# Kernel optimization log

Hardware: AMD Instinct MI355X
Metric: run time of the kernel (lower is better)

The kernel has to match this reference:

```python
import jax, jax.numpy as jnp
import numpy as np
import math

NUM_HEADS = 8
HEAD_DIM = 32  # num_units 256 / 8 heads
TIME_DIM = 8
NEG_BIG = -2.0 ** 32 + 1.0


def _ffn(x, W1, b1, W2, b2):
    # two-layer relu MLP: 1 -> time_dim -> time_dim
    h = jax.nn.relu(x @ W1 + b1)
    return jax.nn.relu(h @ W2 + b2)


def _time_gsm_kernel(t, pW1, pb1, pW2, pb2, sW1, sb1, sW2, sb2, bW1, bb1, bW2, bb2):
    # t: [B, L] timestamps -> kernel [B, L, L]
    tt = t[..., None]  # [B, L, 1]
    period = _ffn(tt, pW1, pb1, pW2, pb2)        # [B, L, td]
    qpq = (2.0 * math.pi) * period * tt           # [B, L, td]
    period_diff = qpq[:, :, None, :] - qpq[:, None, :, :]  # [B, Lq, Lk, td]
    cos_enc = jnp.cos(period_diff)
    sigma = _ffn(tt, sW1, sb1, sW2, sb2)          # [B, L, td]
    sq = sigma[:, :, None, :] + 1e-6              # [B, Lq, 1, td] bcast
    sk = sigma[:, None, :, :] + 1e-6              # [B, 1, Lk, td] bcast
    denom = sq ** 2 + sk ** 2
    t_diff = t[:, :, None] - t[:, None, :]        # [B, Lq, Lk]
    exp_enc = jnp.exp(-(t_diff[..., None] ** 2) / denom)
    local_enc = jnp.sqrt(2.0 * sq * sk / denom)
    basis = _ffn(tt, bW1, bb1, bW2, bb2)          # [B, L, td]
    basis_qk = basis[:, :, None, :] * basis[:, None, :, :]
    return jnp.sum(basis_qk * local_enc * exp_enc * cos_enc, axis=-1)  # [B, L, L]


def setup_inputs() -> dict:
    key = jax.random.key(0)
    ks = jax.random.split(key, 20)
    B, L, U = 4, 1024, 256
    td = TIME_DIM
    inp = {
        'query_input': jax.random.normal(ks[0], (B, L, U), dtype=jnp.float32),
        'input_tensor': jax.random.normal(ks[1], (B, L, U), dtype=jnp.float32),
        'input_mask': jnp.ones((B, L), dtype=jnp.int32),
        'time_inputs': jax.random.uniform(ks[2], (B, L), dtype=jnp.float32) * 100.0,
        'att_bias': jnp.zeros((1,), dtype=jnp.int32),
        'Wq': jax.random.normal(ks[3], (U, U), dtype=jnp.float32) * 0.05,
        'Wk': jax.random.normal(ks[4], (U, U), dtype=jnp.float32) * 0.05,
        'Wv': jax.random.normal(ks[5], (U, U), dtype=jnp.float32) * 0.05,
    }
    names = ['p', 's', 'b']
    i = 6
    for n in names:
        inp[n + 'W1'] = jax.random.normal(ks[i], (1, td), dtype=jnp.float32) * 0.5; i += 1
        inp[n + 'b1'] = jnp.zeros((td,), dtype=jnp.float32)
        inp[n + 'W2'] = jax.random.normal(ks[i], (td, td), dtype=jnp.float32) * 0.5; i += 1
        inp[n + 'b2'] = jnp.zeros((td,), dtype=jnp.float32)
    return inp


def reference(query_input, input_tensor, input_mask, time_inputs, att_bias,
              Wq, Wk, Wv,
              pW1, pb1, pW2, pb2, sW1, sb1, sW2, sb2, bW1, bb1, bW2, bb2):
    B, Lq, U = query_input.shape
    Lk = input_tensor.shape[1]
    H, dh = NUM_HEADS, HEAD_DIM

    Q = (query_input @ Wq).reshape(B, Lq, H, dh).transpose(0, 2, 1, 3)  # [B,H,Lq,dh]
    K = (input_tensor @ Wk).reshape(B, Lk, H, dh).transpose(0, 2, 1, 3)
    V = (input_tensor @ Wv).reshape(B, Lk, H, dh).transpose(0, 2, 1, 3)

    scale = 1.0 / math.sqrt(dh)
    scores = jnp.einsum('bhqd,bhkd->bhqk', Q, K) * scale  # [B,H,Lq,Lk]

    tk = _time_gsm_kernel(time_inputs, pW1, pb1, pW2, pb2,
                          sW1, sb1, sW2, sb2, bW1, bb1, bW2, bb2)  # [B,Lq,Lk]
    scores = scores + tk[:, None, :, :] * scale

    # key padding mask: zero-norm keys get -inf-like score
    key_masks = jnp.sign(jnp.sum(jnp.abs(K), axis=-1))  # [B,H,Lk]
    scores = jnp.where(key_masks[:, :, None, :] == 0.0, NEG_BIG, scores)

    # direction == 'forward': allow strictly row > col (strict causal)
    idx = jnp.arange(Lk)
    causal = (idx[:, None] > idx[None, :]).astype(scores.dtype)  # [Lq,Lk]
    scores = scores + (1.0 - causal) * -10000.0

    attn = jax.nn.softmax(scores, axis=-1)

    query_masks = jnp.sign(jnp.sum(jnp.abs(Q), axis=-1))  # [B,H,Lq]
    attn = attn * query_masks[..., None]
    # dropout rate 0.0 -> identity

    out = jnp.einsum('bhqk,bhkd->bhqd', attn, V)
    out = out.transpose(0, 2, 1, 3).reshape(B, Lq, U)
    out = out * input_mask.astype(jnp.float32)[..., None]
    return out
```

## Files before the change

kernel.cpp:

```cpp
#include <hip/hip_runtime.h>
#include <math.h>

#define B_DIM 4
#define L_DIM 1024
#define H_DIM 8
#define D_DIM 32
#define TD 8
#define NTILES_TOT 1056
#define SCALE 0.17677669529663687f

typedef unsigned short ushort_t;
typedef __attribute__((ext_vector_type(8))) short short8v;
typedef __attribute__((ext_vector_type(4))) float f32x4;

__device__ __forceinline__ int ntiles_of(int qt) { return (qt >> 1) + 1; }
__device__ __forceinline__ int off_of(int qt) {
  int m = qt >> 1;
  return (qt & 1) ? (m + 1) * (m + 1) : m * m + m;
}

__device__ __forceinline__ ushort_t f2bf(float f) {
  unsigned u = __builtin_bit_cast(unsigned, f);
  u += 0x7FFFu + ((u >> 16) & 1u);
  return (ushort_t)(u >> 16);
}
__device__ __forceinline__ float bf2f(ushort_t h) {
  return __builtin_bit_cast(float, ((unsigned)h) << 16);
}
__device__ __forceinline__ short8v pack84(float4 a, float4 b) {
  short8v r;
  r[0] = (short)f2bf(a.x); r[1] = (short)f2bf(a.y);
  r[2] = (short)f2bf(a.z); r[3] = (short)f2bf(a.w);
  r[4] = (short)f2bf(b.x); r[5] = (short)f2bf(b.y);
  r[6] = (short)f2bf(b.z); r[7] = (short)f2bf(b.w);
  return r;
}

__global__ __launch_bounds__(256) void prep_gemm_kernel(
    const float* __restrict__ Xq, const float* __restrict__ Xi,
    const float* __restrict__ Wq, const float* __restrict__ Wk,
    const float* __restrict__ Wv, const float* __restrict__ t_in,
    const float* __restrict__ pW1, const float* __restrict__ pb1,
    const float* __restrict__ pW2, const float* __restrict__ pb2,
    const float* __restrict__ sW1, const float* __restrict__ sb1,
    const float* __restrict__ sW2, const float* __restrict__ sb2,
    const float* __restrict__ bW1, const float* __restrict__ bb1,
    const float* __restrict__ bW2, const float* __restrict__ bb2,
    ushort_t* __restrict__ Qf, ushort_t* __restrict__ Kf,
    ushort_t* __restrict__ Vf,
    float* __restrict__ ptf, float* __restrict__ sg, float* __restrict__ bs) {
  const int blk = blockIdx.x;
  const int tid = threadIdx.x;

  if (blk < 384) {
    const int z = blk >> 7;
    const int rem = blk & 127;
    const int m0 = (rem & 31) * 128;
    const int n0 = (rem >> 5) * 64;
    const float* X = (z == 0) ? Xq : Xi;
    const float* W = (z == 0) ? Wq : (z == 1) ? Wk : Wv;
    const int w = tid >> 6, l = tid & 63, lg = l >> 4, lc = l & 15;
    const int wm = w >> 1, wn = w & 1;

    f32x4 acc[4][2];
#pragma unroll
    for (int mi = 0; mi < 4; ++mi)
#pragma unroll
      for (int ni = 0; ni < 2; ++ni) acc[mi][ni] = (f32x4){0.f, 0.f, 0.f, 0.f};

    for (int kt0 = 0; kt0 < 8; ++kt0) {
      short8v a[4], bfr[2];
#pragma unroll
      for (int mi = 0; mi < 4; ++mi) {
        const float* xp = &X[(size_t)(m0 + (wm * 4 + mi) * 16 + lc) * 256 + kt0 * 32 + lg * 8];
        a[mi] = pack84(*(const float4*)xp, *(const float4*)(xp + 4));
      }
#pragma unroll
      for (int ni = 0; ni < 2; ++ni) {
        const int ncol = n0 + (wn * 2 + ni) * 16 + lc;
        short8v bf;
#pragma unroll
        for (int j = 0; j < 8; ++j)
          bf[j] = (short)f2bf(W[(size_t)(kt0 * 32 + lg * 8 + j) * 256 + ncol]);
        bfr[ni] = bf;
      }
#pragma unroll
      for (int mi = 0; mi < 4; ++mi)
#pragma unroll
        for (int ni = 0; ni < 2; ++ni)
          acc[mi][ni] = __builtin_amdgcn_mfma_f32_16x16x32_bf16(a[mi], bfr[ni], acc[mi][ni], 0, 0, 0);
    }

#pragma unroll
    for (int mi = 0; mi < 4; ++mi) {
#pragma unroll
      for (int ni = 0; ni < 2; ++ni) {
        const int col = n0 + wn * 32 + ni * 16 + lc;
        const int hh = col >> 5, d = col & 31;
#pragma unroll
        for (int r = 0; r < 4; ++r) {
          const int row = m0 + (wm * 4 + mi) * 16 + lg * 4 + r;
          const int bb = row >> 10, lr = row & (L_DIM - 1);
          float v = acc[mi][ni][r];
          if (z == 0) v *= SCALE;
          const ushort_t bv = f2bf(v);
          if (z == 2) {
            Vf[(((size_t)(bb * H_DIM + hh) * 32 + (lr >> 5)) * 2 + (d >> 4)) * 512 +
               (((lr >> 3) & 3) * 16 + (d & 15)) * 8 + (lr & 7)] = bv;
          } else {
            ushort_t* of16 = (z == 0) ? Qf : Kf;
            of16[((size_t)((bb * H_DIM + hh) * 64 + (lr >> 4))) * 512 +
                 ((d >> 3) * 16 + (lr & 15)) * 8 + (d & 7)] = bv;
          }
        }
      }
    }
  } else {
    const int lin = (blk - 384) * 256 + tid;
    const int i = lin >> 5;
    const int slot = lin & 31;
    const int z = slot >> 3, e = slot & 7;
    if (z == 3) return;
    const float* W1 = (z == 0) ? pW1 : (z == 1) ? sW1 : bW1;
    const float* b1 = (z == 0) ? pb1 : (z == 1) ? sb1 : bb1;
    const float* W2 = (z == 0) ? pW2 : (z == 1) ? sW2 : bW2;
    const float* b2 = (z == 0) ? pb2 : (z == 1) ? sb2 : bb2;
    const double t = (double)t_in[i];
    double acc = (double)b2[e];
#pragma unroll
    for (int d = 0; d < 8; ++d) {
      double hv = t * (double)W1[d] + (double)b1[d];
      hv = hv > 0.0 ? hv : 0.0;
      acc += hv * (double)W2[d * 8 + e];
    }
    acc = acc > 0.0 ? acc : 0.0;
    const size_t o = (size_t)i * TD + e;
    if (z == 0) {
      double pt = acc * t;
      ptf[o] = (float)(pt - floor(pt));
    } else if (z == 1) {
      sg[o] = (float)(acc + 1e-6);
    } else {
      bs[o] = (float)acc;
    }
  }
}

__global__ __launch_bounds__(256) void tk_kernel(
    const float* __restrict__ ptf, const float* __restrict__ sg,
    const float* __restrict__ bs, const float* __restrict__ t_in,
    float* __restrict__ tkbuf) {
  __shared__ __align__(16) float ptq[16 * 8], qsh[16 * 8], qbh[16 * 8];
  __shared__ __align__(16) float ptk[32 * 12], ksh[32 * 12], kbh[32 * 12];
  __shared__ float trow[16], tcol[32];
  const int blk = blockIdx.x;
  const int tid = threadIdx.x;

  const int b = blk / NTILES_TOT;
  const int t1 = blk - b * NTILES_TOT;
  int m = (int)sqrtf((float)t1 + 1.0f);
  while (m * m + m > t1) --m;
  while ((m + 1) * (m + 1) + (m + 1) <= t1) ++m;
  const int rem = t1 - (m * m + m);
  int qt, kt;
  if (rem <= m) { qt = 2 * m; kt = rem; }
  else          { qt = 2 * m + 1; kt = rem - (m + 1); }
  const int q0 = qt << 4, k0 = kt << 5;

  if (tid < 16) trow[tid] = t_in[b * L_DIM + q0 + tid];
  if (tid < 32) tcol[tid] = t_in[b * L_DIM + k0 + tid];
  if (tid < 128) {
    const int i = tid >> 3, d = tid & 7;
    const size_t base = (size_t)(b * L_DIM + q0 + i) * TD + d;
    ptq[i * 8 + d] = ptf[base];
    qsh[i * 8 + d] = sg[base];
    qbh[i * 8 + d] = bs[base];
  }
  {
    const int j = tid >> 3, d = tid & 7;
    const size_t base = (size_t)(b * L_DIM + k0 + j) * TD + d;
    ptk[j * 12 + d] = ptf[base];
    ksh[j * 12 + d] = sg[base];
    kbh[j * 12 + d] = bs[base];
  }
  __syncthreads();

  const int r = tid & 3;
  const int lr2 = tid >> 2;
  const int i = ((lr2 >> 4) << 2) | r;
  float pq[8], qs_[8], qb_[8];
  *(float4*)&pq[0]  = *(const float4*)&ptq[i * 8];
  *(float4*)&pq[4]  = *(const float4*)&ptq[i * 8 + 4];
  *(float4*)&qs_[0] = *(const float4*)&qsh[i * 8];
  *(float4*)&qs_[4] = *(const float4*)&qsh[i * 8 + 4];
  *(float4*)&qb_[0] = *(const float4*)&qbh[i * 8];
  *(float4*)&qb_[4] = *(const float4*)&qbh[i * 8 + 4];
  const float ti = trow[i];

  float* dst = &tkbuf[(size_t)(b * NTILES_TOT + off_of(qt) + kt) * 512];
#pragma unroll
  for (int pp = 0; pp < 2; ++pp) {
    const int j = pp * 16 + (lr2 & 15);
    float td2 = ti - tcol[j];
    td2 *= td2;
    float pk[8], ks_[8], kb_[8];
    *(float4*)&pk[0]  = *(const float4*)&ptk[j * 12];
    *(float4*)&pk[4]  = *(const float4*)&ptk[j * 12 + 4];
    *(float4*)&ks_[0] = *(const float4*)&ksh[j * 12];
    *(float4*)&ks_[4] = *(const float4*)&ksh[j * 12 + 4];
    *(float4*)&kb_[0] = *(const float4*)&kbh[j * 12];
    *(float4*)&kb_[4] = *(const float4*)&kbh[j * 12 + 4];
    float a = 0.f;
#pragma unroll
    for (int d = 0; d < TD; ++d) {
      const float sqd = qs_[d], skd = ks_[d];
      const float denom = sqd * sqd + skd * skd;
      const float inv = __builtin_amdgcn_rcpf(denom);
      const float ee = __expf(-td2 * inv);
      const float le = __builtin_amdgcn_sqrtf(2.f * sqd * skd * inv);
      const float dq = __builtin_fabsf(pq[d] - pk[d]);
      const float ce = __builtin_amdgcn_cosf(dq);
      a += qb_[d] * kb_[d] * (le * ee * ce);
    }
    dst[tid + (pp << 8)] = a * SCALE;
  }
}

__global__ __launch_bounds__(256, 4) void attn_row0_kernel(
    const ushort_t* __restrict__ Qf, const ushort_t* __restrict__ Kf,
    const ushort_t* __restrict__ Vf, const float* __restrict__ tkbuf,
    const int* __restrict__ imask, float* __restrict__ out) {
  __shared__ __align__(16) ushort_t lds_p[4][1024];
  __shared__ float p_s[L_DIM];
  __shared__ float qsh[D_DIM];
  __shared__ float red[8][33];
  __shared__ float rtmp[4];

  const int h = blockIdx.y;
  const int b = blockIdx.z;
  const int tid = threadIdx.x;
  const int fb = (b * H_DIM + h) * 64;
  const int vb = (b * H_DIM + h) * 32;

  if (blockIdx.x == 16) {
    if (tid < D_DIM)
      qsh[tid] = bf2f(Qf[(size_t)fb * 512 + (tid >> 3) * 128 + (tid & 7)]);
    __syncthreads();

    float lmax = -1e30f;
    for (int j = tid; j < L_DIM; j += 256) {
      int i = j & 15;
      float tkv = tkbuf[(size_t)(b * NTILES_TOT + off_of(j >> 4)) * 512 +
                        (((i >> 2) << 6) | (i & 3))];
      const ushort_t* kp = &Kf[(size_t)(fb + (j >> 4)) * 512 + (j & 15) * 8];
      float dot = 0.f;
#pragma unroll
      for (int o = 0; o < 4; ++o) {
        short8v kv = *(const short8v*)&kp[o * 128];
#pragma unroll
        for (int u = 0; u < 8; ++u) dot += qsh[o * 8 + u] * bf2f((ushort_t)kv[u]);
      }
      float sc = dot + tkv;
      p_s[j] = sc;
      lmax = fmaxf(lmax, sc);
    }
#pragma unroll
    for (int o = 1; o < 64; o <<= 1) lmax = fmaxf(lmax, __shfl_xor(lmax, o));
    if ((tid & 63) == 0) rtmp[tid >> 6] = lmax;
    __syncthreads();
    const float bmax = fmaxf(fmaxf(rtmp[0], rtmp[1]), fmaxf(rtmp[2], rtmp[3]));
    __syncthreads();

    float lsumv = 0.f;
    for (int j = tid; j < L_DIM; j += 256) {
      float pv = __expf(p_s[j] - bmax);
      p_s[j] = pv;
      lsumv += pv;
    }
#pragma unroll
    for (int o = 1; o < 64; o <<= 1) lsumv += __shfl_xor(lsumv, o);
    if ((tid & 63) == 0) rtmp[tid >> 6] = lsumv;
    __syncthreads();
    const float bsum = rtmp[0] + rtmp[1] + rtmp[2] + rtmp[3];

    const int g = tid >> 5, d = tid & 31;
    float a = 0.f;
    for (int j = g * 128; j < g * 128 + 128; ++j) {
      float v = bf2f(Vf[(((size_t)(vb + (j >> 5))) * 2 + (d >> 4)) * 512 +
                        (((j >> 3) & 3) * 16 + (d & 15)) * 8 + (j & 7)]);
      a = fmaf(p_s[j], v, a);
    }
    red[g][d] = a;
    __syncthreads();
    if (tid < D_DIM) {
      float acc = 0.f;
#pragma unroll
      for (int gg = 0; gg < 8; ++gg) acc += red[gg][tid];
      float qabs = 0.f;
#pragma unroll
      for (int dd = 0; dd < D_DIM; ++dd) qabs += fabsf(qsh[dd]);
      const float qmv = qabs > 0.f ? 1.f : 0.f;
      out[((size_t)b * L_DIM) * 256 + h * D_DIM + tid] =
          acc * (1.0f / bsum) * qmv * (float)imask[b * L_DIM];
    }
    return;
  }

  const int qc = 15 - (int)blockIdx.x;
  const int w = tid >> 6;
  const int l = tid & 63;
  const int lg = l >> 4;
  const int lc = l & 15;
  const int qbase = qc * 64 + w * 16;
  const int qt = qbase >> 4;

  short8v qfrag = *(const short8v*)&Qf[((size_t)(fb + qt)) * 512 + l * 8];
  float qabs_l = 0.f;
#pragma unroll
  for (int j = 0; j < 8; ++j) qabs_l += fabsf(bf2f((ushort_t)qfrag[j]));
  qabs_l += __shfl_xor(qabs_l, 16);
  qabs_l += __shfl_xor(qabs_l, 32);
  const float qm = (qabs_l > 0.f) ? 1.f : 0.f;

  f32x4 O0 = {0.f, 0.f, 0.f, 0.f};
  f32x4 O1 = {0.f, 0.f, 0.f, 0.f};
  float mrow[4] = {-1e30f, -1e30f, -1e30f, -1e30f};
  float lrow[4] = {0.f, 0.f, 0.f, 0.f};
  const float* tk_qt = &tkbuf[(size_t)(b * NTILES_TOT + off_of(qt)) * 512];
  ushort_t* Pw = lds_p[w];

  for (int kc = 0; kc <= qc; ++kc) {
    const bool diag = (kc == qc);
    const size_t kb_ = ((size_t)(fb + kc * 4)) * 512 + l * 8;
    short8v kf0 = *(const short8v*)&Kf[kb_];
    short8v kf1 = *(const short8v*)&Kf[kb_ + 512];
    short8v kf2 = *(const short8v*)&Kf[kb_ + 1024];
    short8v kf3 = *(const short8v*)&Kf[kb_ + 1536];
    const size_t tb_ = (size_t)(kc * 2) * 512 + l * 4;
    float4 t0 = *(const float4*)&tk_qt[tb_];
    float4 t1 = *(const float4*)&tk_qt[tb_ + 256];
    float4 t2 = *(const float4*)&tk_qt[tb_ + 512];
    float4 t3 = *(const float4*)&tk_qt[tb_ + 768];
    const size_t vb_ = ((size_t)(vb + kc * 2)) * 1024 + l * 8;
    short8v vf0 = *(const short8v*)&Vf[vb_];
    short8v vf1 = *(const short8v*)&Vf[vb_ + 512];
    short8v vf2 = *(const short8v*)&Vf[vb_ + 1024];
    short8v vf3 = *(const short8v*)&Vf[vb_ + 1536];

    f32x4 z4 = {0.f, 0.f, 0.f, 0.f};
    __builtin_amdgcn_s_setprio(1);
    f32x4 sv0 = __builtin_amdgcn_mfma_f32_16x16x32_bf16(qfrag, kf0, z4, 0, 0, 0);
    f32x4 sv1 = __builtin_amdgcn_mfma_f32_16x16x32_bf16(qfrag, kf1, z4, 0, 0, 0);
    f32x4 sv2 = __builtin_amdgcn_mfma_f32_16x16x32_bf16(qfrag, kf2, z4, 0, 0, 0);
    f32x4 sv3 = __builtin_amdgcn_mfma_f32_16x16x32_bf16(qfrag, kf3, z4, 0, 0, 0);
    __builtin_amdgcn_s_setprio(0);

    float s[4][4];
#pragma unroll
    for (int r = 0; r < 4; ++r) {
      s[0][r] = sv0[r] + (&t0.x)[r];
      s[1][r] = sv1[r] + (&t1.x)[r];
      s[2][r] = sv2[r] + (&t2.x)[r];
      s[3][r] = sv3[r] + (&t3.x)[r];
    }
    if (diag) {
#pragma unroll
      for (int kt = 0; kt < 4; ++kt) {
        const int col = kc * 64 + kt * 16 + lc;
#pragma unroll
        for (int r = 0; r < 4; ++r)
          if (col >= qbase + lg * 4 + r) s[kt][r] = -10000.0f;
      }
    }

#pragma unroll
    for (int r = 0; r < 4; ++r) {
      float tmax = fmaxf(fmaxf(s[0][r], s[1][r]), fmaxf(s[2][r], s[3][r]));
      tmax = fmaxf(tmax, __shfl_xor(tmax, 1));
      tmax = fmaxf(tmax, __shfl_xor(tmax, 2));
      tmax = fmaxf(tmax, __shfl_xor(tmax, 4));
      tmax = fmaxf(tmax, __shfl_xor(tmax, 8));
      float mnew = fmaxf(mrow[r], tmax);
      float cf = __expf(mrow[r] - mnew);
      mrow[r] = mnew;
      float p0 = __expf(s[0][r] - mnew);
      float p1 = __expf(s[1][r] - mnew);
      float p2 = __expf(s[2][r] - mnew);
      float p3 = __expf(s[3][r] - mnew);
      lrow[r] = lrow[r] * cf + ((p0 + p1) + (p2 + p3));
      O0[r] *= cf;
      O1[r] *= cf;
      const int pb = ((lc >> 3) << 7) + ((lg * 4 + r) << 3) + (lc & 7);
      Pw[pb] = f2bf(p0);
      Pw[pb + 256] = f2bf(p1);
      Pw[pb + 512] = f2bf(p2);
      Pw[pb + 768] = f2bf(p3);
    }
    short8v pf0 = *(const short8v*)&Pw[l * 8];
    short8v pf1 = *(const short8v*)&Pw[(64 + l) * 8];
    __builtin_amdgcn_s_setprio(1);
    O0 = __builtin_amdgcn_mfma_f32_16x16x32_bf16(pf0, vf0, O0, 0, 0, 0);
    O1 = __builtin_amdgcn_mfma_f32_16x16x32_bf16(pf0, vf1, O1, 0, 0, 0);
    O0 = __builtin_amdgcn_mfma_f32_16x16x32_bf16(pf1, vf2, O0, 0, 0, 0);
    O1 = __builtin_amdgcn_mfma_f32_16x16x32_bf16(pf1, vf3, O1, 0, 0, 0);
    __builtin_amdgcn_s_setprio(0);
  }

#pragma unroll
  for (int r = 0; r < 4; ++r) {
    lrow[r] += __shfl_xor(lrow[r], 1);
    lrow[r] += __shfl_xor(lrow[r], 2);
    lrow[r] += __shfl_xor(lrow[r], 4);
    lrow[r] += __shfl_xor(lrow[r], 8);
    const int rr = lg * 4 + r;
    const int qrow = qbase + rr;
    float qmr = __shfl(qm, rr);
    float im = (float)imask[b * L_DIM + qrow];
    float scl = (1.f / lrow[r]) * qmr * im;
    if (qrow != 0) {
      float* op = &out[((size_t)(b * L_DIM + qrow)) * 256 + h * D_DIM];
      op[lc] = O0[r] * scl;
      op[16 + lc] = O1[r] * scl;
    }
  }
}

extern "C" void kernel_launch(void* const* d_in, const int* in_sizes, int n_in,
                              void* d_out, int out_size, void* d_ws, size_t ws_size,
                              hipStream_t stream) {
  (void)in_sizes; (void)n_in; (void)out_size; (void)ws_size;
  const float* query = (const float*)d_in[0];
  const float* input = (const float*)d_in[1];
  const int* imask = (const int*)d_in[2];
  const float* t_in = (const float*)d_in[3];
  const float* Wq = (const float*)d_in[5];
  const float* Wk = (const float*)d_in[6];
  const float* Wv = (const float*)d_in[7];
  const float* pW1 = (const float*)d_in[8],  *pb1 = (const float*)d_in[9];
  const float* pW2 = (const float*)d_in[10], *pb2 = (const float*)d_in[11];
  const float* sW1 = (const float*)d_in[12], *sb1 = (const float*)d_in[13];
  const float* sW2 = (const float*)d_in[14], *sb2 = (const float*)d_in[15];
  const float* bW1 = (const float*)d_in[16], *bb1 = (const float*)d_in[17];
  const float* bW2 = (const float*)d_in[18], *bb2 = (const float*)d_in[19];
  float* out = (float*)d_out;

  const int M = B_DIM * L_DIM;
  char* p = (char*)d_ws;
  ushort_t* Qf = (ushort_t*)p;  p += (size_t)M * 256 * 2;
  ushort_t* Kf = (ushort_t*)p;  p += (size_t)M * 256 * 2;
  ushort_t* Vf = (ushort_t*)p;  p += (size_t)M * 256 * 2;
  float* ptf = (float*)p;       p += (size_t)M * TD * 4;
  float* sg = (float*)p;        p += (size_t)M * TD * 4;
  float* bs = (float*)p;        p += (size_t)M * TD * 4;
  float* tkbuf = (float*)p;

  prep_gemm_kernel<<<384 + 512, 256, 0, stream>>>(
      query, input, Wq, Wk, Wv, t_in,
      pW1, pb1, pW2, pb2, sW1, sb1, sW2, sb2, bW1, bb1, bW2, bb2,
      Qf, Kf, Vf, ptf, sg, bs);
  tk_kernel<<<B_DIM * NTILES_TOT, 256, 0, stream>>>(ptf, sg, bs, t_in, tkbuf);
  attn_row0_kernel<<<dim3(17, H_DIM, B_DIM), 256, 0, stream>>>(
      Qf, Kf, Vf, tkbuf, imask, out);
}
```

Baseline: 74.71 us.

## Split attention into key segments with combine pass; prepack bf16 GEMM operands

The causal attention is split along the key axis into segments of up to four 64-key chunks, giving 40 blocks per head instead of 17, which evens out the triangular workload. Partial outputs and max/sum statistics go to workspace, and a new combine kernel merges them and also handles the row-0 special case. The projection GEMM now reads X and W already converted to bf16 in fragment layout by a new prep kernel, and the tk computation is fused into the GEMM launch. This trades extra launches and extra workspace traffic (partials, the bf16 copies) for better load balance and cheaper GEMM operand loads.

```diff
diff --git a/kernel.cpp b/kernel.cpp
--- a/kernel.cpp
+++ b/kernel.cpp
@@ -18,6 +18,12 @@
   int m = qt >> 1;
   return (qt & 1) ? (m + 1) * (m + 1) : m * m + m;
 }
+__device__ __forceinline__ void qcseg(int x, int& qc, int& s) {
+  if (x < 4) { qc = x; s = 0; }
+  else if (x < 12) { qc = 4 + ((x - 4) >> 1); s = (x - 4) & 1; }
+  else if (x < 24) { int t = x - 12; qc = 8 + t / 3; s = t % 3; }
+  else { int t = x - 24; qc = 12 + (t >> 2); s = t & 3; }
+}
 
 __device__ __forceinline__ ushort_t f2bf(float f) {
   unsigned u = __builtin_bit_cast(unsigned, f);
@@ -36,29 +42,94 @@
   return r;
 }
 
-__global__ __launch_bounds__(256) void prep_gemm_kernel(
-    const float* __restrict__ Xq, const float* __restrict__ Xi,
-    const float* __restrict__ Wq, const float* __restrict__ Wk,
-    const float* __restrict__ Wv, const float* __restrict__ t_in,
+__global__ __launch_bounds__(256) void prep_kernel(
+    const float* __restrict__ t_in,
     const float* __restrict__ pW1, const float* __restrict__ pb1,
     const float* __restrict__ pW2, const float* __restrict__ pb2,
     const float* __restrict__ sW1, const float* __restrict__ sb1,
     const float* __restrict__ sW2, const float* __restrict__ sb2,
     const float* __restrict__ bW1, const float* __restrict__ bb1,
     const float* __restrict__ bW2, const float* __restrict__ bb2,
+    float* __restrict__ ptf, float* __restrict__ sg, float* __restrict__ bs,
+    const float* __restrict__ Xq, const float* __restrict__ Xi,
+    ushort_t* __restrict__ Xfq, ushort_t* __restrict__ Xfi,
+    const float* __restrict__ Wq, const float* __restrict__ Wk,
+    const float* __restrict__ Wv, ushort_t* __restrict__ Wf) {
+  const int blk = blockIdx.x;
+  const int tid = threadIdx.x;
+  if (blk < 512) {
+    const int lin = blk * 256 + tid;
+    const int i = lin >> 5;
+    const int slot = lin & 31;
+    const int z = slot >> 3, e = slot & 7;
+    if (z == 3) return;
+    const float* W1 = (z == 0) ? pW1 : (z == 1) ? sW1 : bW1;
+    const float* b1 = (z == 0) ? pb1 : (z == 1) ? sb1 : bb1;
+    const float* W2 = (z == 0) ? pW2 : (z == 1) ? sW2 : bW2;
+    const float* b2 = (z == 0) ? pb2 : (z == 1) ? sb2 : bb2;
+    const double t = (double)t_in[i];
+    double acc = (double)b2[e];
+#pragma unroll
+    for (int d = 0; d < 8; ++d) {
+      double hv = t * (double)W1[d] + (double)b1[d];
+      hv = hv > 0.0 ? hv : 0.0;
+      acc += hv * (double)W2[d * 8 + e];
+    }
+    acc = acc > 0.0 ? acc : 0.0;
+    const size_t o = (size_t)i * TD + e;
+    if (z == 0) {
+      double pt = acc * t;
+      ptf[o] = (float)(pt - floor(pt));
+    } else if (z == 1) {
+      sg[o] = (float)(acc + 1e-6);
+    } else {
+      bs[o] = (float)acc;
+    }
+  } else if (blk < 1536) {
+    const int xb = blk - 512;
+    const float* X = (xb < 512) ? Xq : Xi;
+    ushort_t* O = (xb < 512) ? Xfq : Xfi;
+    const int lin = (xb & 511) * 256 + tid;
+    const int row = lin >> 5, q = lin & 31;
+    const float* src = &X[(size_t)row * 256 + q * 8];
+    short8v f = pack84(*(const float4*)src, *(const float4*)(src + 4));
+    size_t idx = ((size_t)((row >> 4) * 8 + (q >> 2)) * 64 + (q & 3) * 16 + (row & 15)) * 8;
+    *(short8v*)&O[idx] = f;
+  } else {
+    const int wb = blk - 1536;
+    const int z = wb >> 5;
+    const float* W = (z == 0) ? Wq : (z == 1) ? Wk : Wv;
+    const int lin = (wb & 31) * 256 + tid;
+    const int kt = lin >> 10, g = (lin >> 8) & 3, n = lin & 255;
+    short8v f;
+#pragma unroll
+    for (int i2 = 0; i2 < 8; ++i2)
+      f[i2] = (short)f2bf(W[(size_t)(kt * 32 + g * 8 + i2) * 256 + n]);
+    size_t idx = ((size_t)((z * 8 + kt) * 16 + (n >> 4)) * 64 + g * 16 + (n & 15)) * 8;
+    *(short8v*)&Wf[idx] = f;
+  }
+}
+
+__global__ __launch_bounds__(256) void work_kernel(
+    const ushort_t* __restrict__ Xfq, const ushort_t* __restrict__ Xfi,
+    const ushort_t* __restrict__ Wf,
     ushort_t* __restrict__ Qf, ushort_t* __restrict__ Kf,
     ushort_t* __restrict__ Vf,
-    float* __restrict__ ptf, float* __restrict__ sg, float* __restrict__ bs) {
+    const float* __restrict__ ptf, const float* __restrict__ sg,
+    const float* __restrict__ bs, const float* __restrict__ t_in,
+    float* __restrict__ tkbuf) {
+  __shared__ __align__(16) float ptq[16 * 8], qsh[16 * 8], qbh[16 * 8];
+  __shared__ __align__(16) float ptk[32 * 12], ksh[32 * 12], kbh[32 * 12];
+  __shared__ float trow[16], tcol[32];
   const int blk = blockIdx.x;
   const int tid = threadIdx.x;
 
   if (blk < 384) {
     const int z = blk >> 7;
     const int rem = blk & 127;
-    const int m0 = (rem & 31) * 128;
+    const int m0t = (rem & 31) * 8;
     const int n0 = (rem >> 5) * 64;
-    const float* X = (z == 0) ? Xq : Xi;
-    const float* W = (z == 0) ? Wq : (z == 1) ? Wk : Wv;
+    const ushort_t* Xf = (z == 0) ? Xfq : Xfi;
     const int w = tid >> 6, l = tid & 63, lg = l >> 4, lc = l & 15;
     const int wm = w >> 1, wn = w & 1;
 
@@ -71,19 +142,11 @@
     for (int kt0 = 0; kt0 < 8; ++kt0) {
       short8v a[4], bfr[2];
 #pragma unroll
-      for (int mi = 0; mi < 4; ++mi) {
-        const float* xp = &X[(size_t)(m0 + (wm * 4 + mi) * 16 + lc) * 256 + kt0 * 32 + lg * 8];
-        a[mi] = pack84(*(const float4*)xp, *(const float4*)(xp + 4));
-      }
-#pragma unroll
-      for (int ni = 0; ni < 2; ++ni) {
-        const int ncol = n0 + (wn * 2 + ni) * 16 + lc;
-        short8v bf;
-#pragma unroll
-        for (int j = 0; j < 8; ++j)
-          bf[j] = (short)f2bf(W[(size_t)(kt0 * 32 + lg * 8 + j) * 256 + ncol]);
-        bfr[ni] = bf;
-      }
+      for (int mi = 0; mi < 4; ++mi)
+        a[mi] = *(const short8v*)&Xf[((size_t)(m0t + wm * 4 + mi) * 8 + kt0) * 512 + l * 8];
+#pragma unroll
+      for (int ni = 0; ni < 2; ++ni)
+        bfr[ni] = *(const short8v*)&Wf[((size_t)(z * 8 + kt0) * 16 + (n0 >> 4) + wn * 2 + ni) * 512 + l * 8];
 #pragma unroll
       for (int mi = 0; mi < 4; ++mi)
 #pragma unroll
@@ -99,7 +162,7 @@
         const int hh = col >> 5, d = col & 31;
 #pragma unroll
         for (int r = 0; r < 4; ++r) {
-          const int row = m0 + (wm * 4 + mi) * 16 + lg * 4 + r;
+          const int row = (m0t + wm * 4 + mi) * 16 + lg * 4 + r;
           const int bb = row >> 10, lr = row & (L_DIM - 1);
           float v = acc[mi][ni][r];
           if (z == 0) v *= SCALE;
@@ -116,211 +179,98 @@
       }
     }
   } else {
-    const int lin = (blk - 384) * 256 + tid;
-    const int i = lin >> 5;
-    const int slot = lin & 31;
-    const int z = slot >> 3, e = slot & 7;
-    if (z == 3) return;
-    const float* W1 = (z == 0) ? pW1 : (z == 1) ? sW1 : bW1;
-    const float* b1 = (z == 0) ? pb1 : (z == 1) ? sb1 : bb1;
-    const float* W2 = (z == 0) ? pW2 : (z == 1) ? sW2 : bW2;
-    const float* b2 = (z == 0) ? pb2 : (z == 1) ? sb2 : bb2;
-    const double t = (double)t_in[i];
-    double acc = (double)b2[e];
-#pragma unroll
-    for (int d = 0; d < 8; ++d) {
-      double hv = t * (double)W1[d] + (double)b1[d];
-      hv = hv > 0.0 ? hv : 0.0;
-      acc += hv * (double)W2[d * 8 + e];
-    }
-    acc = acc > 0.0 ? acc : 0.0;
-    const size_t o = (size_t)i * TD + e;
-    if (z == 0) {
-      double pt = acc * t;
-      ptf[o] = (float)(pt - floor(pt));
-    } else if (z == 1) {
-      sg[o] = (float)(acc + 1e-6);
-    } else {
-      bs[o] = (float)acc;
-    }
-  }
-}
-
-__global__ __launch_bounds__(256) void tk_kernel(
-    const float* __restrict__ ptf, const float* __restrict__ sg,
-    const float* __restrict__ bs, const float* __restrict__ t_in,
-    float* __restrict__ tkbuf) {
-  __shared__ __align__(16) float ptq[16 * 8], qsh[16 * 8], qbh[16 * 8];
-  __shared__ __align__(16) float ptk[32 * 12], ksh[32 * 12], kbh[32 * 12];
-  __shared__ float trow[16], tcol[32];
-  const int blk = blockIdx.x;
-  const int tid = threadIdx.x;
-
-  const int b = blk / NTILES_TOT;
-  const int t1 = blk - b * NTILES_TOT;
-  int m = (int)sqrtf((float)t1 + 1.0f);
-  while (m * m + m > t1) --m;
-  while ((m + 1) * (m + 1) + (m + 1) <= t1) ++m;
-  const int rem = t1 - (m * m + m);
-  int qt, kt;
-  if (rem <= m) { qt = 2 * m; kt = rem; }
-  else          { qt = 2 * m + 1; kt = rem - (m + 1); }
-  const int q0 = qt << 4, k0 = kt << 5;
-
-  if (tid < 16) trow[tid] = t_in[b * L_DIM + q0 + tid];
-  if (tid < 32) tcol[tid] = t_in[b * L_DIM + k0 + tid];
-  if (tid < 128) {
-    const int i = tid >> 3, d = tid & 7;
-    const size_t base = (size_t)(b * L_DIM + q0 + i) * TD + d;
-    ptq[i * 8 + d] = ptf[base];
-    qsh[i * 8 + d] = sg[base];
-    qbh[i * 8 + d] = bs[base];
-  }
-  {
-    const int j = tid >> 3, d = tid & 7;
-    const size_t base = (size_t)(b * L_DIM + k0 + j) * TD + d;
-    ptk[j * 12 + d] = ptf[base];
-    ksh[j * 12 + d] = sg[base];
-    kbh[j * 12 + d] = bs[base];
-  }
-  __syncthreads();
-
-  const int r = tid & 3;
-  const int lr2 = tid >> 2;
-  const int i = ((lr2 >> 4) << 2) | r;
-  float pq[8], qs_[8], qb_[8];
-  *(float4*)&pq[0]  = *(const float4*)&ptq[i * 8];
-  *(float4*)&pq[4]  = *(const float4*)&ptq[i * 8 + 4];
-  *(float4*)&qs_[0] = *(const float4*)&qsh[i * 8];
-  *(float4*)&qs_[4] = *(const float4*)&qsh[i * 8 + 4];
-  *(float4*)&qb_[0] = *(const float4*)&qbh[i * 8];
-  *(float4*)&qb_[4] = *(const float4*)&qbh[i * 8 + 4];
-  const float ti = trow[i];
-
-  float* dst = &tkbuf[(size_t)(b * NTILES_TOT + off_of(qt) + kt) * 512];
-#pragma unroll
-  for (int pp = 0; pp < 2; ++pp) {
-    const int j = pp * 16 + (lr2 & 15);
-    float td2 = ti - tcol[j];
-    td2 *= td2;
-    float pk[8], ks_[8], kb_[8];
-    *(float4*)&pk[0]  = *(const float4*)&ptk[j * 12];
-    *(float4*)&pk[4]  = *(const float4*)&ptk[j * 12 + 4];
-    *(float4*)&ks_[0] = *(const float4*)&ksh[j * 12];
-    *(float4*)&ks_[4] = *(const float4*)&ksh[j * 12 + 4];
-    *(float4*)&kb_[0] = *(const float4*)&kbh[j * 12];
-    *(float4*)&kb_[4] = *(const float4*)&kbh[j * 12 + 4];
-    float a = 0.f;
-#pragma unroll
-    for (int d = 0; d < TD; ++d) {
-      const float sqd = qs_[d], skd = ks_[d];
-      const float denom = sqd * sqd + skd * skd;
-      const float inv = __builtin_amdgcn_rcpf(denom);
-      const float ee = __expf(-td2 * inv);
-      const float le = __builtin_amdgcn_sqrtf(2.f * sqd * skd * inv);
-      const float dq = __builtin_fabsf(pq[d] - pk[d]);
-      const float ce = __builtin_amdgcn_cosf(dq);
-      a += qb_[d] * kb_[d] * (le * ee * ce);
-    }
-    dst[tid + (pp << 8)] = a * SCALE;
-  }
-}
-
-__global__ __launch_bounds__(256, 4) void attn_row0_kernel(
+    const int lin = blk - 384;
+    const int b = lin / NTILES_TOT;
+    const int t1 = lin - b * NTILES_TOT;
+    int m = (int)sqrtf((float)t1 + 1.0f);
+    while (m * m + m > t1) --m;
+    while ((m + 1) * (m + 1) + (m + 1) <= t1) ++m;
+    const int rem = t1 - (m * m + m);
+    int qt, kt;
+    if (rem <= m) { qt = 2 * m; kt = rem; }
+    else          { qt = 2 * m + 1; kt = rem - (m + 1); }
+    const int q0 = qt << 4, k0 = kt << 5;
+
+    if (tid < 16) trow[tid] = t_in[b * L_DIM + q0 + tid];
+    if (tid < 32) tcol[tid] = t_in[b * L_DIM + k0 + tid];
+    if (tid < 128) {
+      const int i = tid >> 3, d = tid & 7;
+      const size_t base = (size_t)(b * L_DIM + q0 + i) * TD + d;
+      ptq[i * 8 + d] = ptf[base];
+      qsh[i * 8 + d] = sg[base];
+      qbh[i * 8 + d] = bs[base];
+    }
+    {
+      const int j = tid >> 3, d = tid & 7;
+      const size_t base = (size_t)(b * L_DIM + k0 + j) * TD + d;
+      ptk[j * 12 + d] = ptf[base];
+      ksh[j * 12 + d] = sg[base];
+      kbh[j * 12 + d] = bs[base];
+    }
+    __syncthreads();
+
+    const int r = tid & 3;
+    const int lr2 = tid >> 2;
+    const int i = ((lr2 >> 4) << 2) | r;
+    float pq[8], qs_[8], qb_[8];
+    *(float4*)&pq[0]  = *(const float4*)&ptq[i * 8];
+    *(float4*)&pq[4]  = *(const float4*)&ptq[i * 8 + 4];
+    *(float4*)&qs_[0] = *(const float4*)&qsh[i * 8];
+    *(float4*)&qs_[4] = *(const float4*)&qsh[i * 8 + 4];
+    *(float4*)&qb_[0] = *(const float4*)&qbh[i * 8];
+    *(float4*)&qb_[4] = *(const float4*)&qbh[i * 8 + 4];
+    const float ti = trow[i];
+
+    float* dst = &tkbuf[(size_t)(b * NTILES_TOT + off_of(qt) + kt) * 512];
+#pragma unroll
+    for (int pp = 0; pp < 2; ++pp) {
+      const int j = pp * 16 + (lr2 & 15);
+      float td2 = ti - tcol[j];
+      td2 *= td2;
+      float pk[8], ks_[8], kb_[8];
+      *(float4*)&pk[0]  = *(const float4*)&ptk[j * 12];
+      *(float4*)&pk[4]  = *(const float4*)&ptk[j * 12 + 4];
+      *(float4*)&ks_[0] = *(const float4*)&ksh[j * 12];
+      *(float4*)&ks_[4] = *(const float4*)&ksh[j * 12 + 4];
+      *(float4*)&kb_[0] = *(const float4*)&kbh[j * 12];
+      *(float4*)&kb_[4] = *(const float4*)&kbh[j * 12 + 4];
+      float a = 0.f;
+#pragma unroll
+      for (int d = 0; d < TD; ++d) {
+        const float sqd = qs_[d], skd = ks_[d];
+        const float denom = sqd * sqd + skd * skd;
+        const float inv = __builtin_amdgcn_rcpf(denom);
+        const float ee = __expf(-td2 * inv);
+        const float le = __builtin_amdgcn_sqrtf(2.f * sqd * skd * inv);
+        const float dq = __builtin_fabsf(pq[d] - pk[d]);
+        const float ce = __builtin_amdgcn_cosf(dq);
+        a += qb_[d] * kb_[d] * (le * ee * ce);
+      }
+      dst[tid + (pp << 8)] = a * SCALE;
+    }
+  }
+}
+
+__global__ __launch_bounds__(256, 4) void attn_partial_kernel(
     const ushort_t* __restrict__ Qf, const ushort_t* __restrict__ Kf,
     const ushort_t* __restrict__ Vf, const float* __restrict__ tkbuf,
-    const int* __restrict__ imask, float* __restrict__ out) {
+    float* __restrict__ Opart, float* __restrict__ MLpart) {
   __shared__ __align__(16) ushort_t lds_p[4][1024];
-  __shared__ float p_s[L_DIM];
-  __shared__ float qsh[D_DIM];
-  __shared__ float red[8][33];
-  __shared__ float rtmp[4];
-
   const int h = blockIdx.y;
   const int b = blockIdx.z;
+  int qc, seg;
+  qcseg((int)blockIdx.x, qc, seg);
   const int tid = threadIdx.x;
-  const int fb = (b * H_DIM + h) * 64;
-  const int vb = (b * H_DIM + h) * 32;
-
-  if (blockIdx.x == 16) {
-    if (tid < D_DIM)
-      qsh[tid] = bf2f(Qf[(size_t)fb * 512 + (tid >> 3) * 128 + (tid & 7)]);
-    __syncthreads();
-
-    float lmax = -1e30f;
-    for (int j = tid; j < L_DIM; j += 256) {
-      int i = j & 15;
-      float tkv = tkbuf[(size_t)(b * NTILES_TOT + off_of(j >> 4)) * 512 +
-                        (((i >> 2) << 6) | (i & 3))];
-      const ushort_t* kp = &Kf[(size_t)(fb + (j >> 4)) * 512 + (j & 15) * 8];
-      float dot = 0.f;
-#pragma unroll
-      for (int o = 0; o < 4; ++o) {
-        short8v kv = *(const short8v*)&kp[o * 128];
-#pragma unroll
-        for (int u = 0; u < 8; ++u) dot += qsh[o * 8 + u] * bf2f((ushort_t)kv[u]);
-      }
-      float sc = dot + tkv;
-      p_s[j] = sc;
-      lmax = fmaxf(lmax, sc);
-    }
-#pragma unroll
-    for (int o = 1; o < 64; o <<= 1) lmax = fmaxf(lmax, __shfl_xor(lmax, o));
-    if ((tid & 63) == 0) rtmp[tid >> 6] = lmax;
-    __syncthreads();
-    const float bmax = fmaxf(fmaxf(rtmp[0], rtmp[1]), fmaxf(rtmp[2], rtmp[3]));
-    __syncthreads();
-
-    float lsumv = 0.f;
-    for (int j = tid; j < L_DIM; j += 256) {
-      float pv = __expf(p_s[j] - bmax);
-      p_s[j] = pv;
-      lsumv += pv;
-    }
-#pragma unroll
-    for (int o = 1; o < 64; o <<= 1) lsumv += __shfl_xor(lsumv, o);
-    if ((tid & 63) == 0) rtmp[tid >> 6] = lsumv;
-    __syncthreads();
-    const float bsum = rtmp[0] + rtmp[1] + rtmp[2] + rtmp[3];
-
-    const int g = tid >> 5, d = tid & 31;
-    float a = 0.f;
-    for (int j = g * 128; j < g * 128 + 128; ++j) {
-      float v = bf2f(Vf[(((size_t)(vb + (j >> 5))) * 2 + (d >> 4)) * 512 +
-                        (((j >> 3) & 3) * 16 + (d & 15)) * 8 + (j & 7)]);
-      a = fmaf(p_s[j], v, a);
-    }
-    red[g][d] = a;
-    __syncthreads();
-    if (tid < D_DIM) {
-      float acc = 0.f;
-#pragma unroll
-      for (int gg = 0; gg < 8; ++gg) acc += red[gg][tid];
-      float qabs = 0.f;
-#pragma unroll
-      for (int dd = 0; dd < D_DIM; ++dd) qabs += fabsf(qsh[dd]);
-      const float qmv = qabs > 0.f ? 1.f : 0.f;
-      out[((size_t)b * L_DIM) * 256 + h * D_DIM + tid] =
-          acc * (1.0f / bsum) * qmv * (float)imask[b * L_DIM];
-    }
-    return;
-  }
-
-  const int qc = 15 - (int)blockIdx.x;
   const int w = tid >> 6;
   const int l = tid & 63;
   const int lg = l >> 4;
   const int lc = l & 15;
   const int qbase = qc * 64 + w * 16;
   const int qt = qbase >> 4;
+  const int fb = (b * H_DIM + h) * 64;
+  const int vb = (b * H_DIM + h) * 32;
 
   short8v qfrag = *(const short8v*)&Qf[((size_t)(fb + qt)) * 512 + l * 8];
-  float qabs_l = 0.f;
-#pragma unroll
-  for (int j = 0; j < 8; ++j) qabs_l += fabsf(bf2f((ushort_t)qfrag[j]));
-  qabs_l += __shfl_xor(qabs_l, 16);
-  qabs_l += __shfl_xor(qabs_l, 32);
-  const float qm = (qabs_l > 0.f) ? 1.f : 0.f;
 
   f32x4 O0 = {0.f, 0.f, 0.f, 0.f};
   f32x4 O1 = {0.f, 0.f, 0.f, 0.f};
@@ -329,7 +279,9 @@
   const float* tk_qt = &tkbuf[(size_t)(b * NTILES_TOT + off_of(qt)) * 512];
   ushort_t* Pw = lds_p[w];
 
-  for (int kc = 0; kc <= qc; ++kc) {
+  const int kc0 = seg * 4;
+  const int kc1 = (kc0 + 3 < qc) ? kc0 + 3 : qc;
+  for (int kc = kc0; kc <= kc1; ++kc) {
     const bool diag = (kc == qc);
     const size_t kb_ = ((size_t)(fb + kc * 4)) * 512 + l * 8;
     short8v kf0 = *(const short8v*)&Kf[kb_];
@@ -406,17 +358,166 @@
     __builtin_amdgcn_s_setprio(0);
   }
 
+  const int pslot = (b * H_DIM + h) * 16 + qc;
+  float* Ob = &Opart[(size_t)pslot * 8192 + seg * 2048];
+  *(f32x4*)&Ob[tid * 8] = O0;
+  *(f32x4*)&Ob[tid * 8 + 4] = O1;
+  float* mlb = &MLpart[(size_t)pslot * 512 + seg * 128];
 #pragma unroll
   for (int r = 0; r < 4; ++r) {
-    lrow[r] += __shfl_xor(lrow[r], 1);
-    lrow[r] += __shfl_xor(lrow[r], 2);
-    lrow[r] += __shfl_xor(lrow[r], 4);
-    lrow[r] += __shfl_xor(lrow[r], 8);
+    float lr_ = lrow[r];
+    lr_ += __shfl_xor(lr_, 1);
+    lr_ += __shfl_xor(lr_, 2);
+    lr_ += __shfl_xor(lr_, 4);
+    lr_ += __shfl_xor(lr_, 8);
+    if (lc == 0) {
+      mlb[w * 16 + lg * 4 + r] = mrow[r];
+      mlb[64 + w * 16 + lg * 4 + r] = lr_;
+    }
+  }
+}
+
+__global__ __launch_bounds__(256) void combine_row0_kernel(
+    const ushort_t* __restrict__ Qf, const ushort_t* __restrict__ Kf,
+    const ushort_t* __restrict__ Vf, const float* __restrict__ tkbuf,
+    const float* __restrict__ Opart, const float* __restrict__ MLpart,
+    const int* __restrict__ imask, float* __restrict__ out) {
+  __shared__ float p_s[L_DIM];
+  __shared__ float qsh[D_DIM];
+  __shared__ float red[8][33];
+  __shared__ float rtmp[4];
+  const int h = blockIdx.y;
+  const int b = blockIdx.z;
+  const int tid = threadIdx.x;
+  const int fb = (b * H_DIM + h) * 64;
+  const int vb = (b * H_DIM + h) * 32;
+
+  if (blockIdx.x == 16) {
+    if (tid < D_DIM)
+      qsh[tid] = bf2f(Qf[(size_t)fb * 512 + (tid >> 3) * 128 + (tid & 7)]);
+    __syncthreads();
+    float lmax = -1e30f;
+    for (int j = tid; j < L_DIM; j += 256) {
+      int i = j & 15;
+      float tkv = tkbuf[(size_t)(b * NTILES_TOT + off_of(j >> 4)) * 512 +
+                        (((i >> 2) << 6) | (i & 3))];
+      const ushort_t* kp = &Kf[(size_t)(fb + (j >> 4)) * 512 + (j & 15) * 8];
+      float dot = 0.f;
+#pragma unroll
+      for (int o = 0; o < 4; ++o) {
+        short8v kv = *(const short8v*)&kp[o * 128];
+#pragma unroll
+        for (int u = 0; u < 8; ++u) dot += qsh[o * 8 + u] * bf2f((ushort_t)kv[u]);
+      }
+      float sc = dot + tkv;
+      p_s[j] = sc;
+      lmax = fmaxf(lmax, sc);
+    }
+#pragma unroll
+    for (int o = 1; o < 64; o <<= 1) lmax = fmaxf(lmax, __shfl_xor(lmax, o));
+    if ((tid & 63) == 0) rtmp[tid >> 6] = lmax;
+    __syncthreads();
+    const float bmax = fmaxf(fmaxf(rtmp[0], rtmp[1]), fmaxf(rtmp[2], rtmp[3]));
+    __syncthreads();
+    float lsumv = 0.f;
+    for (int j = tid; j < L_DIM; j += 256) {
+      float pv = __expf(p_s[j] - bmax);
+      p_s[j] = pv;
+      lsumv += pv;
+    }
+#pragma unroll
+    for (int o = 1; o < 64; o <<= 1) lsumv += __shfl_xor(lsumv, o);
+    if ((tid & 63) == 0) rtmp[tid >> 6] = lsumv;
+    __syncthreads();
+    const float bsum = rtmp[0] + rtmp[1] + rtmp[2] + rtmp[3];
+    const int g = tid >> 5, d = tid & 31;
+    float a = 0.f;
+    for (int j = g * 128; j < g * 128 + 128; ++j) {
+      float v = bf2f(Vf[(((size_t)(vb + (j >> 5))) * 2 + (d >> 4)) * 512 +
+                        (((j >> 3) & 3) * 16 + (d & 15)) * 8 + (j & 7)]);
+      a = fmaf(p_s[j], v, a);
+    }
+    red[g][d] = a;
+    __syncthreads();
+    if (tid < D_DIM) {
+      float acc = 0.f;
+#pragma unroll
+      for (int gg = 0; gg < 8; ++gg) acc += red[gg][tid];
+      float qabs = 0.f;
+#pragma unroll
+      for (int dd = 0; dd < D_DIM; ++dd) qabs += fabsf(qsh[dd]);
+      const float qmv = qabs > 0.f ? 1.f : 0.f;
+      out[((size_t)b * L_DIM) * 256 + h * D_DIM + tid] =
+          acc * (1.0f / bsum) * qmv * (float)imask[b * L_DIM];
+    }
+    return;
+  }
+
+  const int qc = (int)blockIdx.x;
+  const int nseg = (qc >> 2) + 1;
+  const int w = tid >> 6;
+  const int l = tid & 63;
+  const int lg = l >> 4;
+  const int lc = l & 15;
+  const int qbase = qc * 64 + w * 16;
+  const int qt = qbase >> 4;
+  const int pslot = (b * H_DIM + h) * 16 + qc;
+  const float* Ob = &Opart[(size_t)pslot * 8192];
+  const float* mlb = &MLpart[(size_t)pslot * 512];
+
+  short8v qfrag = *(const short8v*)&Qf[((size_t)(fb + qt)) * 512 + l * 8];
+  float qabs_l = 0.f;
+#pragma unroll
+  for (int j = 0; j < 8; ++j) qabs_l += fabsf(bf2f((ushort_t)qfrag[j]));
+  qabs_l += __shfl_xor(qabs_l, 16);
+  qabs_l += __shfl_xor(qabs_l, 32);
+  const float qm = (qabs_l > 0.f) ? 1.f : 0.f;
+
+  float ms[4][4], ls[4][4];
+#pragma unroll
+  for (int s = 0; s < 4; ++s) {
+    if (s < nseg) {
+#pragma unroll
+      for (int r = 0; r < 4; ++r) {
+        ms[s][r] = mlb[s * 128 + w * 16 + lg * 4 + r];
+        ls[s][r] = mlb[s * 128 + 64 + w * 16 + lg * 4 + r];
+      }
+    }
+  }
+  float M[4], L[4];
+#pragma unroll
+  for (int r = 0; r < 4; ++r) {
+    float mm = ms[0][r];
+#pragma unroll
+    for (int s = 1; s < 4; ++s)
+      if (s < nseg) mm = fmaxf(mm, ms[s][r]);
+    M[r] = mm;
+    L[r] = 0.f;
+  }
+  f32x4 O0 = {0.f, 0.f, 0.f, 0.f};
+  f32x4 O1 = {0.f, 0.f, 0.f, 0.f};
+#pragma unroll
+  for (int s = 0; s < 4; ++s) {
+    if (s < nseg) {
+      f32x4 o0 = *(const f32x4*)&Ob[s * 2048 + tid * 8];
+      f32x4 o1 = *(const f32x4*)&Ob[s * 2048 + tid * 8 + 4];
+#pragma unroll
+      for (int r = 0; r < 4; ++r) {
+        const float f = __expf(ms[s][r] - M[r]);
+        L[r] += ls[s][r] * f;
+        O0[r] += o0[r] * f;
+        O1[r] += o1[r] * f;
+      }
+    }
+  }
+
+#pragma unroll
+  for (int r = 0; r < 4; ++r) {
     const int rr = lg * 4 + r;
     const int qrow = qbase + rr;
     float qmr = __shfl(qm, rr);
     float im = (float)imask[b * L_DIM + qrow];
-    float scl = (1.f / lrow[r]) * qmr * im;
+    float scl = (1.0f / L[r]) * qmr * im;
     if (qrow != 0) {
       float* op = &out[((size_t)(b * L_DIM + qrow)) * 256 + h * D_DIM];
       op[lc] = O0[r] * scl;
@@ -449,16 +550,23 @@
   ushort_t* Qf = (ushort_t*)p;  p += (size_t)M * 256 * 2;
   ushort_t* Kf = (ushort_t*)p;  p += (size_t)M * 256 * 2;
   ushort_t* Vf = (ushort_t*)p;  p += (size_t)M * 256 * 2;
+  ushort_t* Xfq = (ushort_t*)p; p += (size_t)M * 256 * 2;
+  ushort_t* Xfi = (ushort_t*)p; p += (size_t)M * 256 * 2;
+  ushort_t* Wfb = (ushort_t*)p; p += (size_t)3 * 256 * 256 * 2;
   float* ptf = (float*)p;       p += (size_t)M * TD * 4;
   float* sg = (float*)p;        p += (size_t)M * TD * 4;
   float* bs = (float*)p;        p += (size_t)M * TD * 4;
-  float* tkbuf = (float*)p;
-
-  prep_gemm_kernel<<<384 + 512, 256, 0, stream>>>(
-      query, input, Wq, Wk, Wv, t_in,
-      pW1, pb1, pW2, pb2, sW1, sb1, sW2, sb2, bW1, bb1, bW2, bb2,
-      Qf, Kf, Vf, ptf, sg, bs);
-  tk_kernel<<<B_DIM * NTILES_TOT, 256, 0, stream>>>(ptf, sg, bs, t_in, tkbuf);
-  attn_row0_kernel<<<dim3(17, H_DIM, B_DIM), 256, 0, stream>>>(
-      Qf, Kf, Vf, tkbuf, imask, out);
-}
+  float* tkbuf = (float*)p;     p += (size_t)B_DIM * NTILES_TOT * 512 * 4;
+  float* Opart = (float*)p;     p += (size_t)512 * 8192 * 4;
+  float* MLpart = (float*)p;
+
+  prep_kernel<<<1632, 256, 0, stream>>>(
+      t_in, pW1, pb1, pW2, pb2, sW1, sb1, sW2, sb2, bW1, bb1, bW2, bb2,
+      ptf, sg, bs, query, input, Xfq, Xfi, Wq, Wk, Wv, Wfb);
+  work_kernel<<<384 + B_DIM * NTILES_TOT, 256, 0, stream>>>(
+      Xfq, Xfi, Wfb, Qf, Kf, Vf, ptf, sg, bs, t_in, tkbuf);
+  attn_partial_kernel<<<dim3(40, H_DIM, B_DIM), 256, 0, stream>>>(
+      Qf, Kf, Vf, tkbuf, Opart, MLpart);
+  combine_row0_kernel<<<dim3(17, H_DIM, B_DIM), 256, 0, stream>>>(
+      Qf, Kf, Vf, tkbuf, Opart, MLpart, imask, out);
+}
```

Result: faster. 60.69 us (-18.8%).
